# Performance work log

Measured on AMD Instinct MI355X. Metric: run time of the kernel, lower is better.

## Reference

```python
import jax, jax.numpy as jnp
import numpy as np

D_MODEL = 512
NHEAD = 8
HEAD_DIM = D_MODEL // NHEAD  # 64, also rotary_dim
WIN_LO, WIN_HI = 127, 128    # attn_window: kv in [q-127, q+128]
BLOCK = 256                  # block size for banded attention (>= WIN_LO+1 and >= WIN_HI)


def setup_inputs() -> dict:
    key = jax.random.key(0)
    k1, k2, k3, k4 = jax.random.split(key, 4)
    N, T = 4, 2048
    x = jax.random.normal(k1, (N, T, D_MODEL), dtype=jnp.float32)
    Wqkv_w = jax.random.normal(k2, (3 * D_MODEL, D_MODEL), dtype=jnp.float32) * 0.02
    out_w = jax.random.normal(k3, (D_MODEL, D_MODEL), dtype=jnp.float32) * 0.02
    out_b = jax.random.normal(k4, (D_MODEL,), dtype=jnp.float32) * 0.02
    return {"x": x, "Wqkv_w": Wqkv_w, "out_w": out_w, "out_b": out_b}


def _rotate_half(u):
    u1, u2 = jnp.split(u, 2, axis=-1)
    return jnp.concatenate((-u2, u1), axis=-1)


def _apply_rope(q, k, T, dtype):
    # inv_freq: [HEAD_DIM/2]
    inv_freq = 1.0 / (10000.0 ** (jnp.arange(0, HEAD_DIM, 2, dtype=jnp.float32) / HEAD_DIM))
    pos = jnp.arange(T, dtype=dtype)
    freqs = pos[:, None] * inv_freq[None, :].astype(dtype)      # [T, D/2]
    emb = jnp.concatenate((freqs, freqs), axis=-1)              # [T, D]
    cos = jnp.cos(emb)[None, :, None, :]                        # [1,T,1,D]
    sin = jnp.sin(emb)[None, :, None, :]
    q = q * cos + _rotate_half(q) * sin
    k = k * cos + _rotate_half(k) * sin
    return q, k


def reference(x, Wqkv_w, out_w, out_b):
    N, T, dm = x.shape
    H, D, B = NHEAD, HEAD_DIM, BLOCK
    qkv = (x @ Wqkv_w.T).reshape(N, T, 3, H, D)
    q, k, v = qkv[:, :, 0], qkv[:, :, 1], qkv[:, :, 2]          # [N,T,H,D]
    q, k = _apply_rope(q, k, T, x.dtype)
    # [N,H,T,D]
    q = q.transpose(0, 2, 1, 3)
    k = k.transpose(0, 2, 1, 3)
    v = v.transpose(0, 2, 1, 3)

    nb = T // B
    qb = q.reshape(N, H, nb, B, D)
    kb = k.reshape(N, H, nb, B, D)
    vb = v.reshape(N, H, nb, B, D)
    # pad one block of zeros on each side so block g sees key blocks g-1,g,g+1
    pad = ((0, 0), (0, 0), (1, 1), (0, 0), (0, 0))
    kp = jnp.pad(kb, pad)
    vp = jnp.pad(vb, pad)
    # [N,H,nb,3B,D]
    kwin = jnp.concatenate([kp[:, :, i:i + nb] for i in range(3)], axis=3)
    vwin = jnp.concatenate([vp[:, :, i:i + nb] for i in range(3)], axis=3)

    scale = 1.0 / np.sqrt(D)
    scores = jnp.einsum('nhgqd,nhgkd->nhgqk', qb, kwin) * scale  # [N,H,nb,B,3B]

    qi = jnp.arange(B)
    kj = jnp.arange(3 * B)
    gidx = jnp.arange(nb)
    diff = kj[None, None, :] - B - qi[None, :, None]             # [1,B,3B] kv - q offset
    band = (diff >= -WIN_LO) & (diff <= WIN_HI)
    kv_global = gidx[:, None, None] * B + kj[None, None, :] - B  # [nb,1,3B]
    valid = (kv_global >= 0) & (kv_global < T)
    mask = band & valid                                          # [nb,B,3B]

    neg = jnp.asarray(-1e30, dtype=scores.dtype)
    scores = jnp.where(mask[None, None], scores, neg)
    probs = jax.nn.softmax(scores, axis=-1)
    attn = jnp.einsum('nhgqk,nhgkd->nhgqd', probs, vwin)         # [N,H,nb,B,D]
    attn = attn.reshape(N, H, T, D).transpose(0, 2, 1, 3).reshape(N, T, dm)
    return attn @ out_w.T + out_b
```

## Files before the change

### kernel.cpp

```cpp
#include <hip/hip_runtime.h>
#include <math.h>


typedef __attribute__((ext_vector_type(8))) __bf16 bf16x8;
typedef __attribute__((ext_vector_type(4))) float f32x4;

__device__ __forceinline__ unsigned short f2bf(float f) {
    unsigned int u = __float_as_uint(f);
    u += 0x7fffu + ((u >> 16) & 1u);
    return (unsigned short)(u >> 16);
}
__device__ __forceinline__ unsigned int packbf2(float a, float b) {
    unsigned int ua = __float_as_uint(a); ua += 0x7fffu + ((ua >> 16) & 1u);
    unsigned int ub = __float_as_uint(b); ub += 0x7fffu + ((ub >> 16) & 1u);
    return (ua >> 16) | (ub & 0xffff0000u);
}
__device__ __forceinline__ bf16x8 as_bf16x8(uint4 u) {
    union { uint4 u4; bf16x8 v; } c; c.u4 = u; return c.v;
}
__device__ __forceinline__ bf16x8 ld_frag(const unsigned short* p) {
    return as_bf16x8(*(const uint4*)p);
}

__device__ __forceinline__ void async16(void* lds, const void* g) {
    __builtin_amdgcn_global_load_lds(
        (const __attribute__((address_space(1))) void*)g,
        (__attribute__((address_space(3))) void*)lds,
        16, 0, 0);
}

__global__ __launch_bounds__(256) void cvt_all(
    const float* __restrict__ x, const float* __restrict__ w1,
    const float* __restrict__ w2,
    unsigned short* __restrict__ xb, unsigned short* __restrict__ w1b,
    unsigned short* __restrict__ w2b)
{
    const int n_x  = 8192 * 512 / 4;
    const int n_w1 = 1536 * 512 / 4;
    const int n_w2 = 512 * 512 / 4;
    int i = blockIdx.x * 256 + threadIdx.x;
    const float* in; unsigned short* out; int j;
    if (i < n_x)                    { in = x;  out = xb;  j = i; }
    else if (i < n_x + n_w1)        { in = w1; out = w1b; j = i - n_x; }
    else if (i < n_x + n_w1 + n_w2) { in = w2; out = w2b; j = i - n_x - n_w1; }
    else return;
    float4 v = *(const float4*)(in + 4 * (size_t)j);
    uint2 o;
    o.x = packbf2(v.x, v.y);
    o.y = packbf2(v.z, v.w);
    *(uint2*)(out + 4 * (size_t)j) = o;
}

__global__ __launch_bounds__(256, 5) void gemm_bt_mfma(
    const unsigned short* __restrict__ A, const unsigned short* __restrict__ B,
    const float* __restrict__ bias, void* __restrict__ Cout,
    int M, int O, int K, int write_bf16, int do_rope,
    unsigned short* __restrict__ vT)
{
    __shared__ __align__(16) unsigned short As[128 * 64];
    __shared__ __align__(16) unsigned short Bs[64 * 64];

    const int tid  = threadIdx.x;
    const int wave = tid >> 6;
    const int lane = tid & 63;
    const int l15  = lane & 15;
    const int lg   = lane >> 4;
    const int row0 = blockIdx.x * 128;
    const int col0 = blockIdx.y * 64;
    const int wr   = wave * 32;

    f32x4 acc[2][4] = {};

    const int srow = tid >> 3;
    const int skg  = ((tid & 7) * 8) ^ ((srow & 7) * 8);
    const int fx   = (l15 & 7) * 8;

    for (int k0 = 0; k0 < K; k0 += 64) {
        #pragma unroll
        for (int s = 0; s < 4; ++s)
            async16(&As[(size_t)(s * 256 + tid) * 8],
                    A + (size_t)(row0 + s * 32 + srow) * K + k0 + skg);
        #pragma unroll
        for (int s = 0; s < 2; ++s)
            async16(&Bs[(size_t)(s * 256 + tid) * 8],
                    B + (size_t)(col0 + s * 32 + srow) * K + k0 + skg);
        __syncthreads();

        #pragma unroll
        for (int kstep = 0; kstep < 2; ++kstep) {
            const int kq = (kstep * 32 + lg * 8) ^ fx;
            bf16x8 af[2], bfr[4];
            #pragma unroll
            for (int mt = 0; mt < 2; ++mt)
                af[mt] = ld_frag(&As[(wr + mt * 16 + l15) * 64 + kq]);
            #pragma unroll
            for (int nt = 0; nt < 4; ++nt)
                bfr[nt] = ld_frag(&Bs[(nt * 16 + l15) * 64 + kq]);
            #pragma unroll
            for (int mt = 0; mt < 2; ++mt)
                #pragma unroll
                for (int nt = 0; nt < 4; ++nt)
                    acc[mt][nt] = __builtin_amdgcn_mfma_f32_16x16x32_bf16(
                        af[mt], bfr[nt], acc[mt][nt], 0, 0, 0);
        }
        __syncthreads();
    }

    const int qrow = lg * 4;

    if (do_rope && col0 < 1024) {
        const float cfreq = 0.28782313662425574f;
        const float invf0 = __expf(-(float)l15 * cfreq);
        const float invf1 = __expf(-(float)(16 + l15) * cfreq);
        #pragma unroll
        for (int mt = 0; mt < 2; ++mt) {
            #pragma unroll
            for (int r = 0; r < 4; ++r) {
                const int t = (row0 + wr + mt * 16 + qrow + r) & 2047;
                #pragma unroll
                for (int p = 0; p < 2; ++p) {
                    float ang = (float)t * (p ? invf1 : invf0);
                    float s, c;
                    __sincosf(ang, &s, &c);
                    float a = acc[mt][p][r];
                    float b = acc[mt][p + 2][r];
                    acc[mt][p][r]     = a * c - b * s;
                    acc[mt][p + 2][r] = b * c + a * s;
                }
            }
        }
        if (col0 < 512) {
            #pragma unroll
            for (int mt = 0; mt < 2; ++mt)
                #pragma unroll
                for (int nt = 0; nt < 4; ++nt)
                    #pragma unroll
                    for (int r = 0; r < 4; ++r)
                        acc[mt][nt][r] *= 0.125f;
        }
    }

    if (do_rope && col0 >= 1024) {
        #pragma unroll
        for (int nt = 0; nt < 4; ++nt) {
            const int local = col0 - 1024 + nt * 16 + l15;
            const int hh = local >> 6;
            const int dd = local & 63;
            #pragma unroll
            for (int mt = 0; mt < 2; ++mt) {
                const int rowb = row0 + wr + mt * 16 + qrow;
                const int nn = rowb >> 11;
                const int tt = rowb & 2047;
                uint2 o;
                o.x = packbf2(acc[mt][nt][0], acc[mt][nt][1]);
                o.y = packbf2(acc[mt][nt][2], acc[mt][nt][3]);
                *(uint2*)(vT + ((size_t)(nn * 8 + hh) * 64 + dd) * 2048 + tt) = o;
            }
        }
        return;
    }

    #pragma unroll
    for (int nt = 0; nt < 4; ++nt) {
        const int col = col0 + nt * 16 + l15;
        const float bv = bias ? bias[col] : 0.f;
        #pragma unroll
        for (int mt = 0; mt < 2; ++mt) {
            const int rowb = row0 + wr + mt * 16 + qrow;
            if (write_bf16) {
                unsigned short* C = (unsigned short*)Cout;
                #pragma unroll
                for (int r = 0; r < 4; ++r)
                    C[(size_t)(rowb + r) * O + col] = f2bf(acc[mt][nt][r] + bv);
            } else {
                float* C = (float*)Cout;
                #pragma unroll
                for (int r = 0; r < 4; ++r)
                    C[(size_t)(rowb + r) * O + col] = acc[mt][nt][r] + bv;
            }
        }
    }
}

__global__ __launch_bounds__(256) void attn_mfma_kernel(
    const unsigned short* __restrict__ qkv,
    const unsigned short* __restrict__ vT,
    unsigned short* __restrict__ attnout)
{
    __shared__ __align__(16) unsigned short Kt[64 * 72];
    __shared__ __align__(16) unsigned short Vt[64 * 72];
    __shared__ __align__(16) unsigned short Ps[4][16 * 72];

    const int qt = blockIdx.x;
    const int h  = blockIdx.y;
    const int n  = blockIdx.z;
    const int t0 = qt * 64;
    const int tid  = threadIdx.x;
    const int wave = tid >> 6;
    const int lane = tid & 63;
    const int l15  = lane & 15;
    const int lg   = lane >> 4;
    const int qrow = lg * 4;

    const size_t base = (size_t)n * 2048 * 1536 + (size_t)h * 64;
    const unsigned short* vTh = vT + (size_t)(n * 8 + h) * 64 * 2048;

    bf16x8 qfrag[2];
    {
        const unsigned short* qp = qkv + base + (size_t)(t0 + wave * 16 + l15) * 1536;
        qfrag[0] = ld_frag(qp + lg * 8);
        qfrag[1] = ld_frag(qp + 32 + lg * 8);
    }

    const int skey = tid >> 2;
    const int sd0  = (tid & 3) * 16;

    const int qq = wave * 16 + l15;
    float m_v = -1e30f, l_v = 0.f;
    f32x4 acc_o[4] = {};

    for (int dt = -2; dt <= 2; ++dt) {
        const int kt = qt + dt;
        if (kt < 0 || kt > 31) continue;
        const int s0 = kt * 64;

        {
            const unsigned short* kp = qkv + base + 512 + (size_t)(s0 + skey) * 1536 + sd0;
            *(uint4*)&Kt[skey * 72 + sd0]     = *(const uint4*)kp;
            *(uint4*)&Kt[skey * 72 + sd0 + 8] = *(const uint4*)(kp + 8);

            const unsigned short* vp = vTh + (size_t)skey * 2048 + s0 + sd0;
            *(uint4*)&Vt[skey * 72 + sd0]     = *(const uint4*)vp;
            *(uint4*)&Vt[skey * 72 + sd0 + 8] = *(const uint4*)(vp + 8);
        }
        __syncthreads();

        f32x4 acc_s[4] = {};
        #pragma unroll
        for (int kstep = 0; kstep < 2; ++kstep) {
            #pragma unroll
            for (int nt = 0; nt < 4; ++nt) {
                if ((dt == -2 && nt < wave) || (dt == 2 && nt > wave)) continue;
                bf16x8 kf = ld_frag(&Kt[(nt * 16 + l15) * 72 + kstep * 32 + lg * 8]);
                acc_s[nt] = __builtin_amdgcn_mfma_f32_16x16x32_bf16(
                    kf, qfrag[kstep], acc_s[nt], 0, 0, 0);
            }
        }

        float p[4][4];
        float tm = -1e30f;
        #pragma unroll
        for (int nt = 0; nt < 4; ++nt) {
            #pragma unroll
            for (int r = 0; r < 4; ++r) {
                const int diff = dt * 64 + nt * 16 + qrow + r - qq;
                const bool ok = (diff >= -127) && (diff <= 128);
                const float v = ok ? acc_s[nt][r] : -1e30f;
                p[nt][r] = v;
                tm = fmaxf(tm, v);
            }
        }
        tm = fmaxf(tm, __shfl_xor(tm, 16, 64));
        tm = fmaxf(tm, __shfl_xor(tm, 32, 64));
        const float m_new = fmaxf(m_v, tm);
        const float alpha = __expf(m_v - m_new);
        float psum = 0.f;
        #pragma unroll
        for (int nt = 0; nt < 4; ++nt) {
            #pragma unroll
            for (int r = 0; r < 4; ++r) {
                const float e = __expf(p[nt][r] - m_new);
                p[nt][r] = e;
                psum += e;
            }
        }
        psum += __shfl_xor(psum, 16, 64);
        psum += __shfl_xor(psum, 32, 64);
        l_v = l_v * alpha + psum;
        m_v = m_new;

        #pragma unroll
        for (int r = 0; r < 4; ++r) {
            const float a_r = __shfl(alpha, (lane & 48) + qrow + r, 64);
            #pragma unroll
            for (int nt = 0; nt < 4; ++nt) acc_o[nt][r] *= a_r;
        }

        #pragma unroll
        for (int nt = 0; nt < 4; ++nt) {
            uint2 o;
            o.x = packbf2(p[nt][0], p[nt][1]);
            o.y = packbf2(p[nt][2], p[nt][3]);
            *(uint2*)&Ps[wave][l15 * 72 + nt * 16 + qrow] = o;
        }

        bf16x8 pfrag[2];
        pfrag[0] = ld_frag(&Ps[wave][l15 * 72 + lg * 8]);
        pfrag[1] = ld_frag(&Ps[wave][l15 * 72 + 32 + lg * 8]);

        #pragma unroll
        for (int kstep = 0; kstep < 2; ++kstep) {
            #pragma unroll
            for (int nt = 0; nt < 4; ++nt) {
                bf16x8 vf = ld_frag(&Vt[(nt * 16 + l15) * 72 + kstep * 32 + lg * 8]);
                acc_o[nt] = __builtin_amdgcn_mfma_f32_16x16x32_bf16(
                    pfrag[kstep], vf, acc_o[nt], 0, 0, 0);
            }
        }
        __syncthreads();
    }

    const float linv = 1.0f / l_v;
    float inv_l[4];
    #pragma unroll
    for (int r = 0; r < 4; ++r)
        inv_l[r] = __shfl(linv, (lane & 48) + qrow + r, 64);

    #pragma unroll
    for (int r = 0; r < 4; ++r) {
        const int tq = t0 + wave * 16 + qrow + r;
        unsigned short* op = attnout + (size_t)(n * 2048 + tq) * 512 + h * 64;
        #pragma unroll
        for (int nt = 0; nt < 4; ++nt)
            op[nt * 16 + l15] = f2bf(acc_o[nt][r] * inv_l[r]);
    }
}

extern "C" void kernel_launch(void* const* d_in, const int* in_sizes, int n_in,
                              void* d_out, int out_size, void* d_ws, size_t ws_size,
                              hipStream_t stream)
{
    (void)in_sizes; (void)n_in; (void)out_size; (void)ws_size;

    const float* x     = (const float*)d_in[0];
    const float* Wqkv  = (const float*)d_in[1];
    const float* out_w = (const float*)d_in[2];
    const float* out_b = (const float*)d_in[3];
    float* out = (float*)d_out;

    unsigned short* qkvb  = (unsigned short*)d_ws;
    unsigned short* attnb = qkvb + (size_t)8192 * 1536;
    unsigned short* xb    = attnb + (size_t)8192 * 512;
    unsigned short* wqkvb = xb + (size_t)8192 * 512;
    unsigned short* outwb = wqkvb + (size_t)1536 * 512;
    unsigned short* vTb   = outwb + (size_t)512 * 512;

    cvt_all<<<5120, 256, 0, stream>>>(x, Wqkv, out_w, xb, wqkvb, outwb);

    gemm_bt_mfma<<<dim3(64, 24), 256, 0, stream>>>(xb, wqkvb, nullptr, qkvb,
                                                   8192, 1536, 512, 1, 1, vTb);
    attn_mfma_kernel<<<dim3(32, 8, 4), 256, 0, stream>>>(qkvb, vTb, attnb);
    gemm_bt_mfma<<<dim3(64, 8), 256, 0, stream>>>(attnb, outwb, out_b, out,
                                                  8192, 512, 512, 0, 0, nullptr);
}
```

Baseline: 127.2 us.

## Widen attention blocks to 128 queries and skip fully masked key tiles per wave

The attention kernel now processes 128 query rows per block with 8 waves instead of 64 rows with 4 waves, so each loaded K/V tile is shared by twice as many queries and the total K/V tile loads drop. Each wave computes its band offset and skips the whole softmax/PV step, or individual MFMA sub-tiles, when the key tile falls outside its window. The cost is half as many blocks (512), larger blocks, and more waves idling at barriers on tiles they skip.

```diff
diff --git a/kernel.cpp b/kernel.cpp
--- a/kernel.cpp
+++ b/kernel.cpp
@@ -182,129 +182,133 @@
     }
 }
 
-__global__ __launch_bounds__(256) void attn_mfma_kernel(
+__global__ __launch_bounds__(512) void attn_mfma_kernel(
     const unsigned short* __restrict__ qkv,
     const unsigned short* __restrict__ vT,
     unsigned short* __restrict__ attnout)
 {
     __shared__ __align__(16) unsigned short Kt[64 * 72];
     __shared__ __align__(16) unsigned short Vt[64 * 72];
-    __shared__ __align__(16) unsigned short Ps[4][16 * 72];
-
-    const int qt = blockIdx.x;
-    const int h  = blockIdx.y;
-    const int n  = blockIdx.z;
-    const int t0 = qt * 64;
+    __shared__ __align__(16) unsigned short Ps[8][16 * 72];
+
+    const int qtb = blockIdx.x;
+    const int h   = blockIdx.y;
+    const int n   = blockIdx.z;
+    const int t0  = qtb * 128;
     const int tid  = threadIdx.x;
     const int wave = tid >> 6;
     const int lane = tid & 63;
     const int l15  = lane & 15;
     const int lg   = lane >> 4;
     const int qrow = lg * 4;
+    const int wb   = wave * 16;
 
     const size_t base = (size_t)n * 2048 * 1536 + (size_t)h * 64;
     const unsigned short* vTh = vT + (size_t)(n * 8 + h) * 64 * 2048;
 
     bf16x8 qfrag[2];
     {
-        const unsigned short* qp = qkv + base + (size_t)(t0 + wave * 16 + l15) * 1536;
+        const unsigned short* qp = qkv + base + (size_t)(t0 + wb + l15) * 1536;
         qfrag[0] = ld_frag(qp + lg * 8);
         qfrag[1] = ld_frag(qp + 32 + lg * 8);
     }
 
-    const int skey = tid >> 2;
-    const int sd0  = (tid & 3) * 16;
-
-    const int qq = wave * 16 + l15;
+    const int skey = tid >> 3;
+    const int sd0  = (tid & 7) * 8;
+
     float m_v = -1e30f, l_v = 0.f;
     f32x4 acc_o[4] = {};
 
-    for (int dt = -2; dt <= 2; ++dt) {
-        const int kt = qt + dt;
-        if (kt < 0 || kt > 31) continue;
-        const int s0 = kt * 64;
+    const int jlo = (qtb == 0) ? 2 : 0;
+    const int jhi = (qtb == 15) ? 3 : 5;
+
+    for (int j = jlo; j <= jhi; ++j) {
+        const int s0 = t0 + (j - 2) * 64;
 
         {
             const unsigned short* kp = qkv + base + 512 + (size_t)(s0 + skey) * 1536 + sd0;
-            *(uint4*)&Kt[skey * 72 + sd0]     = *(const uint4*)kp;
-            *(uint4*)&Kt[skey * 72 + sd0 + 8] = *(const uint4*)(kp + 8);
-
+            *(uint4*)&Kt[skey * 72 + sd0] = *(const uint4*)kp;
             const unsigned short* vp = vTh + (size_t)skey * 2048 + s0 + sd0;
-            *(uint4*)&Vt[skey * 72 + sd0]     = *(const uint4*)vp;
-            *(uint4*)&Vt[skey * 72 + sd0 + 8] = *(const uint4*)(vp + 8);
+            *(uint4*)&Vt[skey * 72 + sd0] = *(const uint4*)vp;
         }
         __syncthreads();
 
-        f32x4 acc_s[4] = {};
-        #pragma unroll
-        for (int kstep = 0; kstep < 2; ++kstep) {
+        const int A0 = (j - 2) * 64 - wb;
+        if (A0 > -192 && A0 < 144) {
+            f32x4 acc_s[4] = {};
+            #pragma unroll
+            for (int kstep = 0; kstep < 2; ++kstep) {
+                #pragma unroll
+                for (int nt = 0; nt < 4; ++nt) {
+                    const int D = A0 + nt * 16;
+                    if (D <= -144 || D >= 144) continue;
+                    bf16x8 kf = ld_frag(&Kt[(nt * 16 + l15) * 72 + kstep * 32 + lg * 8]);
+                    acc_s[nt] = __builtin_amdgcn_mfma_f32_16x16x32_bf16(
+                        kf, qfrag[kstep], acc_s[nt], 0, 0, 0);
+                }
+            }
+
+            float p[4][4];
+            float tm = -1e30f;
             #pragma unroll
             for (int nt = 0; nt < 4; ++nt) {
-                if ((dt == -2 && nt < wave) || (dt == 2 && nt > wave)) continue;
-                bf16x8 kf = ld_frag(&Kt[(nt * 16 + l15) * 72 + kstep * 32 + lg * 8]);
-                acc_s[nt] = __builtin_amdgcn_mfma_f32_16x16x32_bf16(
-                    kf, qfrag[kstep], acc_s[nt], 0, 0, 0);
-            }
-        }
-
-        float p[4][4];
-        float tm = -1e30f;
-        #pragma unroll
-        for (int nt = 0; nt < 4; ++nt) {
+                #pragma unroll
+                for (int r = 0; r < 4; ++r) {
+                    const int diff = A0 + nt * 16 + qrow + r - l15;
+                    const bool ok = (diff >= -127) && (diff <= 128);
+                    const float v = ok ? acc_s[nt][r] : -1e30f;
+                    p[nt][r] = v;
+                    tm = fmaxf(tm, v);
+                }
+            }
+            tm = fmaxf(tm, __shfl_xor(tm, 16, 64));
+            tm = fmaxf(tm, __shfl_xor(tm, 32, 64));
+            const float m_new = fmaxf(m_v, tm);
+            const float alpha = __expf(m_v - m_new);
+            float psum = 0.f;
+            #pragma unroll
+            for (int nt = 0; nt < 4; ++nt) {
+                #pragma unroll
+                for (int r = 0; r < 4; ++r) {
+                    const float e = __expf(p[nt][r] - m_new);
+                    p[nt][r] = e;
+                    psum += e;
+                }
+            }
+            psum += __shfl_xor(psum, 16, 64);
+            psum += __shfl_xor(psum, 32, 64);
+            l_v = l_v * alpha + psum;
+            m_v = m_new;
+
             #pragma unroll
             for (int r = 0; r < 4; ++r) {
-                const int diff = dt * 64 + nt * 16 + qrow + r - qq;
-                const bool ok = (diff >= -127) && (diff <= 128);
-                const float v = ok ? acc_s[nt][r] : -1e30f;
-                p[nt][r] = v;
-                tm = fmaxf(tm, v);
-            }
-        }
-        tm = fmaxf(tm, __shfl_xor(tm, 16, 64));
-        tm = fmaxf(tm, __shfl_xor(tm, 32, 64));
-        const float m_new = fmaxf(m_v, tm);
-        const float alpha = __expf(m_v - m_new);
-        float psum = 0.f;
-        #pragma unroll
-        for (int nt = 0; nt < 4; ++nt) {
-            #pragma unroll
-            for (int r = 0; r < 4; ++r) {
-                const float e = __expf(p[nt][r] - m_new);
-                p[nt][r] = e;
-                psum += e;
-            }
-        }
-        psum += __shfl_xor(psum, 16, 64);
-        psum += __shfl_xor(psum, 32, 64);
-        l_v = l_v * alpha + psum;
-        m_v = m_new;
-
-        #pragma unroll
-        for (int r = 0; r < 4; ++r) {
-            const float a_r = __shfl(alpha, (lane & 48) + qrow + r, 64);
-            #pragma unroll
-            for (int nt = 0; nt < 4; ++nt) acc_o[nt][r] *= a_r;
-        }
-
-        #pragma unroll
-        for (int nt = 0; nt < 4; ++nt) {
-            uint2 o;
-            o.x = packbf2(p[nt][0], p[nt][1]);
-            o.y = packbf2(p[nt][2], p[nt][3]);
-            *(uint2*)&Ps[wave][l15 * 72 + nt * 16 + qrow] = o;
-        }
-
-        bf16x8 pfrag[2];
-        pfrag[0] = ld_frag(&Ps[wave][l15 * 72 + lg * 8]);
-        pfrag[1] = ld_frag(&Ps[wave][l15 * 72 + 32 + lg * 8]);
-
-        #pragma unroll
-        for (int kstep = 0; kstep < 2; ++kstep) {
+                const float a_r = __shfl(alpha, (lane & 48) + qrow + r, 64);
+                #pragma unroll
+                for (int nt = 0; nt < 4; ++nt) acc_o[nt][r] *= a_r;
+            }
+
             #pragma unroll
             for (int nt = 0; nt < 4; ++nt) {
-                bf16x8 vf = ld_frag(&Vt[(nt * 16 + l15) * 72 + kstep * 32 + lg * 8]);
-                acc_o[nt] = __builtin_amdgcn_mfma_f32_16x16x32_bf16(
-                    pfrag[kstep], vf, acc_o[nt], 0, 0, 0);
+                uint2 o;
+                o.x = packbf2(p[nt][0], p[nt][1]);
+                o.y = packbf2(p[nt][2], p[nt][3]);
+                *(uint2*)&Ps[wave][l15 * 72 + nt * 16 + qrow] = o;
+            }
+
+            bf16x8 pfrag[2];
+            pfrag[0] = ld_frag(&Ps[wave][l15 * 72 + lg * 8]);
+            pfrag[1] = ld_frag(&Ps[wave][l15 * 72 + 32 + lg * 8]);
+
+            #pragma unroll
+            for (int kstep = 0; kstep < 2; ++kstep) {
+                const int D32 = A0 + kstep * 32;
+                if (D32 <= -176 || D32 >= 144) continue;
+                #pragma unroll
+                for (int nt = 0; nt < 4; ++nt) {
+                    bf16x8 vf = ld_frag(&Vt[(nt * 16 + l15) * 72 + kstep * 32 + lg * 8]);
+                    acc_o[nt] = __builtin_amdgcn_mfma_f32_16x16x32_bf16(
+                        pfrag[kstep], vf, acc_o[nt], 0, 0, 0);
+                }
             }
         }
         __syncthreads();
@@ -318,7 +322,7 @@
 
     #pragma unroll
     for (int r = 0; r < 4; ++r) {
-        const int tq = t0 + wave * 16 + qrow + r;
+        const int tq = t0 + wb + qrow + r;
         unsigned short* op = attnout + (size_t)(n * 2048 + tq) * 512 + h * 64;
         #pragma unroll
         for (int nt = 0; nt < 4; ++nt)
@@ -349,7 +353,7 @@
 
     gemm_bt_mfma<<<dim3(64, 24), 256, 0, stream>>>(xb, wqkvb, nullptr, qkvb,
                                                    8192, 1536, 512, 1, 1, vTb);
-    attn_mfma_kernel<<<dim3(32, 8, 4), 256, 0, stream>>>(qkvb, vTb, attnb);
+    attn_mfma_kernel<<<dim3(16, 8, 4), 512, 0, stream>>>(qkvb, vTb, attnb);
     gemm_bt_mfma<<<dim3(64, 8), 256, 0, stream>>>(attnb, outwb, out_b, out,
                                                   8192, 512, 512, 0, 0, nullptr);
 }
```

Result: no change. 129.1 us (+1.4%).
